# Kernel optimization log

Measured on AMD Instinct MI355X. Metric: run time of the kernel, lower is better.

## Reference

```python
import jax, jax.numpy as jnp
import numpy as np
from jax import lax

C_IN = 256
C_OUT = 256
KS = 3


def _conv(x, w, b):
    # x: [B,C,H,W], w: [O,I,kh,kw] -> NCHW 'SAME' conv, stride 1
    y = lax.conv_general_dilated(x, w, window_strides=(1, 1), padding='SAME',
                                 dimension_numbers=('NCHW', 'OIHW', 'NCHW'))
    return y + b[None, :, None, None]


def setup_inputs() -> dict:
    key = jax.random.key(0)
    ks = jax.random.split(key, 7)
    B, H, W = 2, 64, 64
    fan = C_IN * KS * KS
    lim = float(np.sqrt(6.0 / (fan + C_OUT * KS * KS)))  # xavier uniform
    return {
        'x': jax.random.normal(ks[0], (B, C_IN, H, W), jnp.float32),
        'ref_x': jax.random.normal(ks[1], (B, C_IN, H, W), jnp.float32),
        'conv1_w': jax.random.uniform(ks[2], (C_OUT, C_IN, KS, KS), jnp.float32, -lim, lim),
        'conv1_b': jnp.zeros((C_OUT,), jnp.float32),
        'conv2_w': jax.random.uniform(ks[3], (C_OUT, C_IN, KS, KS), jnp.float32, -lim, lim),
        'conv2_b': jnp.zeros((C_OUT,), jnp.float32),
        'gamma': jnp.array([0.5], jnp.float32),
    }


def reference(x, ref_x, conv1_w, conv1_b, conv2_w, conv2_b, gamma):
    B, Cin, H, W = x.shape
    HW = H * W
    x_f = jax.nn.relu(_conv(x, conv1_w, conv1_b)).reshape(B, C_OUT, HW)        # [B,C,HW]
    r_f = jax.nn.relu(_conv(ref_x, conv1_w, conv1_b))                          # [B,C,H,W]
    r_f = r_f.transpose(0, 2, 3, 1).reshape(B, HW, C_OUT)                      # [B,HW,C]
    corr = jnp.einsum('bnc,bcm->bnm', r_f, x_f)                                # [B,HW,HW]
    corr = jax.nn.softmax(corr, axis=1)                                        # softmax over ref positions
    ref_c2 = jax.nn.relu(_conv(x, conv2_w, conv2_b)).reshape(B, C_OUT, HW)     # [B,C,HW]
    A = jnp.einsum('bcn,bnm->bcm', ref_c2, corr).reshape(x.shape)              # [B,C,H,W]
    return A * gamma[0] + x
```

## Files before the change

### kernel.cpp

```cpp
#include <hip/hip_runtime.h>
#include <hip/hip_bf16.h>

#define B_ 2
#define C_ 256
#define H_ 64
#define W_ 64
#define N_ 4096

typedef short bf16x8 __attribute__((ext_vector_type(8)));
typedef _Float16 f16x8 __attribute__((ext_vector_type(8)));
typedef float f32x4 __attribute__((ext_vector_type(4)));

static __device__ __forceinline__ unsigned short f2bf(float f) {
    union { float f; unsigned u; } uf; uf.f = f;
    unsigned r = uf.u + 0x7fffu + ((uf.u >> 16) & 1u);
    return (unsigned short)(r >> 16);
}
static __device__ __forceinline__ unsigned short f2h_u(float f) {
    union { _Float16 h; unsigned short u; } c; c.h = (_Float16)f; return c.u;
}

static __device__ __forceinline__ void gload16(const void* g, void* l) {
    __builtin_amdgcn_global_load_lds(
        (const __attribute__((address_space(1))) unsigned int*)g,
        (__attribute__((address_space(3))) unsigned int*)l, 16, 0, 0);
}

__global__ __launch_bounds__(256) void cvt_x_k(const float* __restrict__ x,
                                               const float* __restrict__ ref_x,
                                               unsigned short* __restrict__ xtx,
                                               unsigned short* __restrict__ xtr)
{
    __shared__ unsigned short t[64][72];
    const int pt = blockIdx.x, ct = blockIdx.y;
    const int which = blockIdx.z >> 1, b = blockIdx.z & 1;
    const float* in = which ? ref_x : x;
    unsigned short* out = which ? xtr : xtx;
    const int a = threadIdx.x & 63, r = threadIdx.x >> 6;
    #pragma unroll
    for (int i = 0; i < 16; ++i) {
        int c = i * 4 + r;
        t[c][a] = f2h_u(in[((size_t)(b * C_ + ct * 64 + c) << 12) + pt * 64 + a]);
    }
    __syncthreads();
    #pragma unroll
    for (int i = 0; i < 16; ++i) {
        int p = i * 4 + r;
        out[((size_t)(b * N_ + pt * 64 + p) << 8) + ct * 64 + a] = t[a][p];
    }
}

__global__ __launch_bounds__(256) void cvt_w_k(const float* __restrict__ w1,
                                               const float* __restrict__ w2,
                                               unsigned short* __restrict__ wh1,
                                               unsigned short* __restrict__ wh2)
{
    int g = blockIdx.x;
    const float* w = (g < 2304) ? w1 : w2;
    unsigned short* wh = (g < 2304) ? wh1 : wh2;
    int i = (g % 2304) * 256 + threadIdx.x;
    int ci = i & 255, co = (i >> 8) & 255, tap = i >> 16;
    wh[i] = f2h_u(w[((size_t)(co * 256 + ci)) * 9 + tap]);
}

__global__ __launch_bounds__(256) void conv_mfma_k(
    const unsigned short* __restrict__ xtx, const unsigned short* __restrict__ xtr,
    const unsigned short* __restrict__ w1h, const unsigned short* __restrict__ w2h,
    const float* __restrict__ b1, const float* __restrict__ b2,
    unsigned short* __restrict__ f1x, unsigned short* __restrict__ f1r,
    unsigned short* __restrict__ f2)
{
    __shared__ unsigned short As[4 * 576 * 8];
    __shared__ unsigned short Bs[4 * 66 * 32];
    const int tid = threadIdx.x;
    const int pt  = blockIdx.x;
    const int cot = blockIdx.y;
    const int cid = blockIdx.z >> 1;
    const int b   = blockIdx.z & 1;

    const unsigned short* xt = (cid == 1) ? xtr : xtx;
    const unsigned short* wt = (cid == 2) ? w2h : w1h;
    const float* bias = (cid == 2) ? b2 : b1;
    unsigned short* out = (cid == 0) ? f1x : (cid == 1) ? f1r : f2;
    const int trans = (cid != 2);

    const int lane = tid & 63, wid = tid >> 6;
    const int wco = wid >> 1, wpos = wid & 1;
    const int rl = lane & 15, q = lane >> 4;
    const int r0 = pt * 2;

    f32x4 acc[2][4];
    #pragma unroll
    for (int mi = 0; mi < 2; ++mi)
        #pragma unroll
        for (int ni = 0; ni < 4; ++ni)
            #pragma unroll
            for (int e = 0; e < 4; ++e) acc[mi][ni][e] = 0.f;

    for (int k0 = 0; k0 < C_; k0 += 32) {
        #pragma unroll
        for (int tap = 0; tap < 9; ++tap) {
            gload16(wt + ((size_t)(tap * C_ + cot * 64 + lane) << 8) + k0 + wid * 8,
                    &As[(wid * 576 + tap * 64 + lane) * 8]);
        }
        #pragma unroll
        for (int j = 0; j < 5; ++j) {
            int it = tid + j * 256;
            if (it < 1056) {
                int col = it >> 4, sub = it & 15;
                int row = sub >> 2, qb = sub & 3;
                int h = r0 + row - 1, c = col - 1;
                float4 v; v.x = 0.f; v.y = 0.f; v.z = 0.f; v.w = 0.f;
                if (h >= 0 && h < 64 && c >= 0 && c < 64)
                    v = *(const float4*)(xt + ((size_t)(b * N_ + h * 64 + c) << 8) + k0 + qb * 8);
                int chunk = qb ^ ((col >> 1) & 3);
                *(float4*)&Bs[(row * 66 + col) * 32 + chunk * 8] = v;
            }
        }
        __syncthreads();

        #pragma unroll
        for (int tap = 0; tap < 9; ++tap) {
            const int kh = tap / 3, kw = tap % 3;
            f16x8 a0 = *(const f16x8*)&As[(q * 576 + tap * 64 + wco * 32 + rl) * 8];
            f16x8 a1 = *(const f16x8*)&As[(q * 576 + tap * 64 + wco * 32 + 16 + rl) * 8];
            const int chunkB = q ^ (((rl + kw) >> 1) & 3);
            const int rowB = (wpos + kh) * 66;
            #pragma unroll
            for (int ni = 0; ni < 4; ++ni) {
                int colB = ni * 16 + rl + kw;
                f16x8 bf = *(const f16x8*)&Bs[(rowB + colB) * 32 + chunkB * 8];
                acc[0][ni] = __builtin_amdgcn_mfma_f32_16x16x32_f16(a0, bf, acc[0][ni], 0, 0, 0);
                acc[1][ni] = __builtin_amdgcn_mfma_f32_16x16x32_f16(a1, bf, acc[1][ni], 0, 0, 0);
            }
        }
        __syncthreads();
    }

    #pragma unroll
    for (int mi = 0; mi < 2; ++mi) {
        const int co = cot * 64 + wco * 32 + mi * 16 + q * 4;
        float bs[4];
        #pragma unroll
        for (int rr = 0; rr < 4; ++rr) bs[rr] = bias[co + rr];
        #pragma unroll
        for (int ni = 0; ni < 4; ++ni) {
            const int pos = pt * 128 + wpos * 64 + ni * 16 + rl;
            if (trans) {
                unsigned short pk[4];
                #pragma unroll
                for (int rr = 0; rr < 4; ++rr)
                    pk[rr] = f2bf(fmaxf(acc[mi][ni][rr] + bs[rr], 0.f));
                uint2 u;
                u.x = (unsigned)pk[0] | ((unsigned)pk[1] << 16);
                u.y = (unsigned)pk[2] | ((unsigned)pk[3] << 16);
                *(uint2*)&out[((size_t)(b * N_ + pos) << 8) + co] = u;
            } else {
                #pragma unroll
                for (int rr = 0; rr < 4; ++rr)
                    out[((size_t)(b * C_ + co + rr) << 12) + pos] =
                        f2bf(fmaxf(acc[mi][ni][rr] + bs[rr], 0.f));
            }
        }
    }
}

__global__ __launch_bounds__(256) void gemm_corr_k(
    const unsigned short* __restrict__ f1x, const unsigned short* __restrict__ f1r,
    float* __restrict__ corr)
{
    __shared__ alignas(16) unsigned short As[128 * 32];
    __shared__ alignas(16) unsigned short Bs[128 * 32];
    const int tid = threadIdx.x;
    const int tn = blockIdx.x, tm = blockIdx.y, b = blockIdx.z;

    const unsigned short* Ab = f1x + ((size_t)b * N_ + (size_t)tm * 128) * C_;
    const unsigned short* Bb = f1r + ((size_t)b * N_ + (size_t)tn * 128) * C_;

    const int wid = tid >> 6, lane = tid & 63;
    const int wr = wid >> 1, wc = wid & 1;
    const int rl = lane & 15, q = lane >> 4;
    const int srow = wid * 32 + (lane >> 2), sq = lane & 3;

    f32x4 acc[4][4];
    #pragma unroll
    for (int mi = 0; mi < 4; ++mi)
        #pragma unroll
        for (int ni = 0; ni < 4; ++ni)
            #pragma unroll
            for (int e = 0; e < 4; ++e) acc[mi][ni][e] = 0.f;

    for (int k0 = 0; k0 < C_; k0 += 32) {
        gload16(&Ab[(size_t)srow * C_ + k0 + sq * 8],        &As[srow * 32 + sq * 8]);
        gload16(&Ab[(size_t)(srow + 16) * C_ + k0 + sq * 8], &As[(srow + 16) * 32 + sq * 8]);
        gload16(&Bb[(size_t)srow * C_ + k0 + sq * 8],        &Bs[srow * 32 + sq * 8]);
        gload16(&Bb[(size_t)(srow + 16) * C_ + k0 + sq * 8], &Bs[(srow + 16) * 32 + sq * 8]);
        __syncthreads();
        bf16x8 a[4], bb[4];
        #pragma unroll
        for (int mi = 0; mi < 4; ++mi)
            a[mi] = *(const bf16x8*)&As[(wr * 64 + mi * 16 + rl) * 32 + q * 8];
        #pragma unroll
        for (int ni = 0; ni < 4; ++ni)
            bb[ni] = *(const bf16x8*)&Bs[(wc * 64 + ni * 16 + rl) * 32 + q * 8];
        #pragma unroll
        for (int mi = 0; mi < 4; ++mi)
            #pragma unroll
            for (int ni = 0; ni < 4; ++ni)
                acc[mi][ni] = __builtin_amdgcn_mfma_f32_16x16x32_bf16(a[mi], bb[ni], acc[mi][ni], 0, 0, 0);
        __syncthreads();
    }

    #pragma unroll
    for (int mi = 0; mi < 4; ++mi)
        #pragma unroll
        for (int ni = 0; ni < 4; ++ni)
            #pragma unroll
            for (int rr = 0; rr < 4; ++rr) {
                int m = tm * 128 + wr * 64 + mi * 16 + q * 4 + rr;
                int n = tn * 128 + wc * 64 + ni * 16 + rl;
                corr[((size_t)b * N_ + m) * N_ + n] = acc[mi][ni][rr];
            }
}

__global__ __launch_bounds__(256) void softmax_rows_k(float* __restrict__ corr)
{
    __shared__ float red[4];
    const int m = blockIdx.x, b = blockIdx.y;
    float* row = corr + ((size_t)b * N_ + m) * N_;
    float4* row4 = (float4*)row;
    const int tid = threadIdx.x;
    const int wid = tid >> 6, lane = tid & 63;

    float4 v[4];
    float mx = -3.0e38f;
    #pragma unroll
    for (int j = 0; j < 4; ++j) {
        v[j] = row4[tid + j * 256];
        mx = fmaxf(mx, fmaxf(fmaxf(v[j].x, v[j].y), fmaxf(v[j].z, v[j].w)));
    }
    #pragma unroll
    for (int off = 32; off; off >>= 1) mx = fmaxf(mx, __shfl_xor(mx, off));
    if (lane == 0) red[wid] = mx;
    __syncthreads();
    mx = fmaxf(fmaxf(red[0], red[1]), fmaxf(red[2], red[3]));
    __syncthreads();

    float s = 0.f;
    #pragma unroll
    for (int j = 0; j < 4; ++j) {
        v[j].x = __expf(v[j].x - mx);
        v[j].y = __expf(v[j].y - mx);
        v[j].z = __expf(v[j].z - mx);
        v[j].w = __expf(v[j].w - mx);
        s += v[j].x + v[j].y + v[j].z + v[j].w;
    }
    #pragma unroll
    for (int off = 32; off; off >>= 1) s += __shfl_xor(s, off);
    if (lane == 0) red[wid] = s;
    __syncthreads();
    s = red[0] + red[1] + red[2] + red[3];
    const float inv = 1.f / s;

    unsigned short* rb = (unsigned short*)row;
    #pragma unroll
    for (int j = 0; j < 4; ++j) {
        uint2 u;
        u.x = (unsigned)f2bf(v[j].x * inv) | ((unsigned)f2bf(v[j].y * inv) << 16);
        u.y = (unsigned)f2bf(v[j].z * inv) | ((unsigned)f2bf(v[j].w * inv) << 16);
        *(uint2*)&rb[4 * (tid + j * 256)] = u;
    }
}

__global__ __launch_bounds__(512) void gemm_out_k(
    const unsigned short* __restrict__ f2, float* __restrict__ corr)
{
    __shared__ alignas(16) unsigned short As[128 * 32];
    __shared__ alignas(16) unsigned short Bs[128 * 32];
    const int tid = threadIdx.x;
    const int tm = blockIdx.x;
    const int tc = blockIdx.y >> 2;
    const int s  = blockIdx.y & 3;
    const int b  = blockIdx.z;

    const unsigned short* Ab = f2 + ((size_t)b * C_ + (size_t)tc * 128) * N_;
    const unsigned short* Bb = (const unsigned short*)corr
                             + ((size_t)b * N_ + (size_t)tm * 128) * 8192;

    const int wid = tid >> 6, lane = tid & 63;
    const int wc = wid >> 2, wm = wid & 3;
    const int rl = lane & 15, q = lane >> 4;
    const int srow = wid * 16 + (lane >> 2), sq = lane & 3;
    const int nbase = s * 1024;

    f32x4 acc[4][2];
    #pragma unroll
    for (int mi = 0; mi < 4; ++mi)
        #pragma unroll
        for (int ni = 0; ni < 2; ++ni)
            #pragma unroll
            for (int e = 0; e < 4; ++e) acc[mi][ni][e] = 0.f;

    for (int kk = 0; kk < 32; ++kk) {
        const int k0 = nbase + kk * 32;
        gload16(&Ab[(size_t)srow * N_ + k0 + sq * 8],   &As[srow * 32 + sq * 8]);
        gload16(&Bb[(size_t)srow * 8192 + k0 + sq * 8], &Bs[srow * 32 + sq * 8]);
        __syncthreads();
        bf16x8 a[4], bb[2];
        #pragma unroll
        for (int mi = 0; mi < 4; ++mi)
            a[mi] = *(const bf16x8*)&As[(wc * 64 + mi * 16 + rl) * 32 + q * 8];
        #pragma unroll
        for (int ni = 0; ni < 2; ++ni)
            bb[ni] = *(const bf16x8*)&Bs[(wm * 32 + ni * 16 + rl) * 32 + q * 8];
        #pragma unroll
        for (int mi = 0; mi < 4; ++mi)
            #pragma unroll
            for (int ni = 0; ni < 2; ++ni)
                acc[mi][ni] = __builtin_amdgcn_mfma_f32_16x16x32_bf16(a[mi], bb[ni], acc[mi][ni], 0, 0, 0);
        __syncthreads();
    }

    #pragma unroll
    for (int mi = 0; mi < 4; ++mi)
        #pragma unroll
        for (int ni = 0; ni < 2; ++ni)
            #pragma unroll
            for (int rr = 0; rr < 4; ++rr) {
                int c = tc * 128 + wc * 64 + mi * 16 + q * 4 + rr;
                int m = tm * 128 + wm * 32 + ni * 16 + rl;
                size_t e = (((size_t)(s * 2 + b) * C_ + c) << 12) + m;
                corr[(e >> 11) * 4096 + 2048 + (e & 2047)] = acc[mi][ni][rr];
            }
}

__global__ __launch_bounds__(256) void reduce_k(
    const float* __restrict__ corr, const float* __restrict__ x,
    const float* __restrict__ gamma, float* __restrict__ out)
{
    const float g = gamma[0];
    size_t i = (size_t)blockIdx.x * 256 + threadIdx.x;
    size_t idx = i << 2;
    float4 sum; sum.x = 0.f; sum.y = 0.f; sum.z = 0.f; sum.w = 0.f;
    #pragma unroll
    for (int sp = 0; sp < 4; ++sp) {
        size_t e = (size_t)sp * 2097152 + idx;
        float4 v = *(const float4*)&corr[(e >> 11) * 4096 + 2048 + (e & 2047)];
        sum.x += v.x; sum.y += v.y; sum.z += v.z; sum.w += v.w;
    }
    float4 xv = ((const float4*)x)[i];
    float4 o;
    o.x = sum.x * g + xv.x;
    o.y = sum.y * g + xv.y;
    o.z = sum.z * g + xv.z;
    o.w = sum.w * g + xv.w;
    ((float4*)out)[i] = o;
}

extern "C" void kernel_launch(void* const* d_in, const int* in_sizes, int n_in,
                              void* d_out, int out_size, void* d_ws, size_t ws_size,
                              hipStream_t stream) {
    const float* x     = (const float*)d_in[0];
    const float* ref_x = (const float*)d_in[1];
    const float* w1    = (const float*)d_in[2];
    const float* b1    = (const float*)d_in[3];
    const float* w2    = (const float*)d_in[4];
    const float* b2    = (const float*)d_in[5];
    const float* gamma = (const float*)d_in[6];
    float* out = (float*)d_out;

    char* ws = (char*)d_ws;
    size_t off = 0;
    auto nxt = [&](size_t bytes) {
        char* p = ws + off;
        off += (bytes + 255) & ~(size_t)255;
        return p;
    };
    unsigned short* f1x = (unsigned short*)nxt((size_t)B_ * N_ * C_ * 2);
    unsigned short* f1r = (unsigned short*)nxt((size_t)B_ * N_ * C_ * 2);
    unsigned short* f2  = (unsigned short*)nxt((size_t)B_ * N_ * C_ * 2);
    unsigned short* xtx = (unsigned short*)nxt((size_t)B_ * N_ * C_ * 2);
    unsigned short* xtr = (unsigned short*)nxt((size_t)B_ * N_ * C_ * 2);
    unsigned short* w1h = (unsigned short*)nxt((size_t)9 * C_ * C_ * 2);
    unsigned short* w2h = (unsigned short*)nxt((size_t)9 * C_ * C_ * 2);
    float* corr = (float*)nxt((size_t)B_ * N_ * N_ * 4);

    cvt_x_k<<<dim3(64, 4, 4), 256, 0, stream>>>(x, ref_x, xtx, xtr);
    cvt_w_k<<<4608, 256, 0, stream>>>(w1, w2, w1h, w2h);

    conv_mfma_k<<<dim3(32, 4, 6), 256, 0, stream>>>(xtx, xtr, w1h, w2h, b1, b2,
                                                    f1x, f1r, f2);

    gemm_corr_k<<<dim3(32, 32, B_), 256, 0, stream>>>(f1x, f1r, corr);
    softmax_rows_k<<<dim3(N_, B_), 256, 0, stream>>>(corr);
    gemm_out_k<<<dim3(32, 8, B_), 512, 0, stream>>>(f2, corr);
    reduce_k<<<2048, 256, 0, stream>>>(corr, x, gamma, out);
}
```

Baseline: 162.3 us.

## Fuse correlation, softmax and output GEMM into flash-attention kernel with split-K combine

Replaces the separate correlation GEMM, row softmax and output GEMM, which go through a large materialized correlation matrix, with one flash-style kernel. It computes S=K·Q tiles, keeps an online max and sum, and accumulates P·V in registers over split ranges of reference positions. A combine kernel merges the partial outputs using their max and sum statistics and applies gamma and the residual. This removes the B·N·N fp32 round trips through HBM. In exchange it adds per-tile exp work and partial buffers, and has only 512 blocks with non-async LDS staging.

New measurement: 150.5 us. 1.08x faster.

```diff
diff --git a/kernel.cpp b/kernel.cpp
--- a/kernel.cpp
+++ b/kernel.cpp
@@ -10,6 +10,7 @@
 typedef short bf16x8 __attribute__((ext_vector_type(8)));
 typedef _Float16 f16x8 __attribute__((ext_vector_type(8)));
 typedef float f32x4 __attribute__((ext_vector_type(4)));
+typedef float f32x16 __attribute__((ext_vector_type(16)));
 
 static __device__ __forceinline__ unsigned short f2bf(float f) {
     union { float f; unsigned u; } uf; uf.f = f;
@@ -165,195 +166,165 @@
     }
 }
 
-__global__ __launch_bounds__(256) void gemm_corr_k(
-    const unsigned short* __restrict__ f1x, const unsigned short* __restrict__ f1r,
-    float* __restrict__ corr)
-{
-    __shared__ alignas(16) unsigned short As[128 * 32];
-    __shared__ alignas(16) unsigned short Bs[128 * 32];
+__global__ __launch_bounds__(256, 2) void flash_k(
+    const unsigned short* __restrict__ f1x,
+    const unsigned short* __restrict__ f1r,
+    const unsigned short* __restrict__ f2,
+    float* __restrict__ part,
+    float* __restrict__ stats)
+{
+    __shared__ unsigned short Ks[64 * 264];
+    __shared__ unsigned short Vs[256 * 72];
     const int tid = threadIdx.x;
-    const int tn = blockIdx.x, tm = blockIdx.y, b = blockIdx.z;
-
-    const unsigned short* Ab = f1x + ((size_t)b * N_ + (size_t)tm * 128) * C_;
-    const unsigned short* Bb = f1r + ((size_t)b * N_ + (size_t)tn * 128) * C_;
-
-    const int wid = tid >> 6, lane = tid & 63;
-    const int wr = wid >> 1, wc = wid & 1;
-    const int rl = lane & 15, q = lane >> 4;
-    const int srow = wid * 32 + (lane >> 2), sq = lane & 3;
-
-    f32x4 acc[4][4];
-    #pragma unroll
-    for (int mi = 0; mi < 4; ++mi)
-        #pragma unroll
-        for (int ni = 0; ni < 4; ++ni)
+    const int mt = blockIdx.x, s = blockIdx.y, b = blockIdx.z;
+    const int m0 = mt * 32;
+    const int lane = tid & 63, wid = tid >> 6;
+    const int wn = wid & 1, wc2 = wid >> 1;
+    const int rl = lane & 31, l5 = lane >> 5;
+    const int c0w = wc2 * 128;
+    const int nw = wn * 32;
+
+    bf16x8 Qf[16];
+    #pragma unroll
+    for (int st = 0; st < 16; ++st)
+        Qf[st] = *(const bf16x8*)&f1x[(((size_t)b * N_ + m0 + rl) << 8) + st * 16 + l5 * 8];
+
+    f32x16 O[4];
+    #pragma unroll
+    for (int cf = 0; cf < 4; ++cf)
+        #pragma unroll
+        for (int e = 0; e < 16; ++e) O[cf][e] = 0.f;
+    float m_run = -1e30f, l_run = 0.f;
+
+    const int nbase = s * 2048;
+    for (int r = 0; r < 32; ++r) {
+        const int n0 = nbase + r * 64;
+        #pragma unroll
+        for (int j = 0; j < 8; ++j) {
+            int it = tid + j * 256;
+            int n = it >> 5, cq = it & 31;
+            *(float4*)&Ks[n * 264 + cq * 8] =
+                *(const float4*)&f1r[(((size_t)b * N_ + n0 + n) << 8) + cq * 8];
+        }
+        #pragma unroll
+        for (int j = 0; j < 8; ++j) {
+            int it = tid + j * 256;
+            int c = it >> 3, nq = it & 7;
+            *(float4*)&Vs[c * 72 + nq * 8] =
+                *(const float4*)&f2[(((size_t)b * C_ + c) << 12) + n0 + nq * 8];
+        }
+        __syncthreads();
+
+        f32x16 S;
+        #pragma unroll
+        for (int e = 0; e < 16; ++e) S[e] = 0.f;
+        #pragma unroll
+        for (int st = 0; st < 16; ++st) {
+            bf16x8 Kf = *(const bf16x8*)&Ks[(nw + rl) * 264 + st * 16 + l5 * 8];
+            S = __builtin_amdgcn_mfma_f32_32x32x16_bf16(Kf, Qf[st], S, 0, 0, 0);
+        }
+
+        float mx = S[0];
+        #pragma unroll
+        for (int e = 1; e < 16; ++e) mx = fmaxf(mx, S[e]);
+        mx = fmaxf(mx, __shfl_xor(mx, 32));
+        float m_new = fmaxf(m_run, mx);
+        float sc = __expf(m_run - m_new);
+        float p[16]; float lsum = 0.f;
+        #pragma unroll
+        for (int e = 0; e < 16; ++e) { p[e] = __expf(S[e] - m_new); lsum += p[e]; }
+        l_run = l_run * sc + lsum;
+        m_run = m_new;
+        #pragma unroll
+        for (int cf = 0; cf < 4; ++cf)
             #pragma unroll
-            for (int e = 0; e < 4; ++e) acc[mi][ni][e] = 0.f;
-
-    for (int k0 = 0; k0 < C_; k0 += 32) {
-        gload16(&Ab[(size_t)srow * C_ + k0 + sq * 8],        &As[srow * 32 + sq * 8]);
-        gload16(&Ab[(size_t)(srow + 16) * C_ + k0 + sq * 8], &As[(srow + 16) * 32 + sq * 8]);
-        gload16(&Bb[(size_t)srow * C_ + k0 + sq * 8],        &Bs[srow * 32 + sq * 8]);
-        gload16(&Bb[(size_t)(srow + 16) * C_ + k0 + sq * 8], &Bs[(srow + 16) * 32 + sq * 8]);
+            for (int e = 0; e < 16; ++e) O[cf][e] *= sc;
+
+        unsigned pk_[8], xk[8];
+        #pragma unroll
+        for (int g = 0; g < 8; ++g)
+            pk_[g] = (unsigned)f2bf(p[2 * g]) | ((unsigned)f2bf(p[2 * g + 1]) << 16);
+        #pragma unroll
+        for (int g = 0; g < 8; ++g) xk[g] = (unsigned)__shfl_xor((int)pk_[g], 32);
+        union { unsigned d[4]; bf16x8 v; } P0, P1;
+        P0.d[0] = l5 ? xk[2] : pk_[0];
+        P0.d[1] = l5 ? xk[3] : pk_[1];
+        P0.d[2] = l5 ? pk_[2] : xk[0];
+        P0.d[3] = l5 ? pk_[3] : xk[1];
+        P1.d[0] = l5 ? xk[6] : pk_[4];
+        P1.d[1] = l5 ? xk[7] : pk_[5];
+        P1.d[2] = l5 ? pk_[6] : xk[4];
+        P1.d[3] = l5 ? pk_[7] : xk[5];
+
+        #pragma unroll
+        for (int cf = 0; cf < 4; ++cf) {
+            const int vrow = (c0w + cf * 32 + rl) * 72;
+            bf16x8 Vf0 = *(const bf16x8*)&Vs[vrow + nw + l5 * 8];
+            O[cf] = __builtin_amdgcn_mfma_f32_32x32x16_bf16(Vf0, P0.v, O[cf], 0, 0, 0);
+            bf16x8 Vf1 = *(const bf16x8*)&Vs[vrow + nw + 16 + l5 * 8];
+            O[cf] = __builtin_amdgcn_mfma_f32_32x32x16_bf16(Vf1, P1.v, O[cf], 0, 0, 0);
+        }
         __syncthreads();
-        bf16x8 a[4], bb[4];
-        #pragma unroll
-        for (int mi = 0; mi < 4; ++mi)
-            a[mi] = *(const bf16x8*)&As[(wr * 64 + mi * 16 + rl) * 32 + q * 8];
-        #pragma unroll
-        for (int ni = 0; ni < 4; ++ni)
-            bb[ni] = *(const bf16x8*)&Bs[(wc * 64 + ni * 16 + rl) * 32 + q * 8];
-        #pragma unroll
-        for (int mi = 0; mi < 4; ++mi)
-            #pragma unroll
-            for (int ni = 0; ni < 4; ++ni)
-                acc[mi][ni] = __builtin_amdgcn_mfma_f32_16x16x32_bf16(a[mi], bb[ni], acc[mi][ni], 0, 0, 0);
-        __syncthreads();
-    }
-
-    #pragma unroll
-    for (int mi = 0; mi < 4; ++mi)
-        #pragma unroll
-        for (int ni = 0; ni < 4; ++ni)
-            #pragma unroll
-            for (int rr = 0; rr < 4; ++rr) {
-                int m = tm * 128 + wr * 64 + mi * 16 + q * 4 + rr;
-                int n = tn * 128 + wc * 64 + ni * 16 + rl;
-                corr[((size_t)b * N_ + m) * N_ + n] = acc[mi][ni][rr];
-            }
-}
-
-__global__ __launch_bounds__(256) void softmax_rows_k(float* __restrict__ corr)
-{
-    __shared__ float red[4];
-    const int m = blockIdx.x, b = blockIdx.y;
-    float* row = corr + ((size_t)b * N_ + m) * N_;
-    float4* row4 = (float4*)row;
-    const int tid = threadIdx.x;
-    const int wid = tid >> 6, lane = tid & 63;
-
-    float4 v[4];
-    float mx = -3.0e38f;
-    #pragma unroll
-    for (int j = 0; j < 4; ++j) {
-        v[j] = row4[tid + j * 256];
-        mx = fmaxf(mx, fmaxf(fmaxf(v[j].x, v[j].y), fmaxf(v[j].z, v[j].w)));
-    }
-    #pragma unroll
-    for (int off = 32; off; off >>= 1) mx = fmaxf(mx, __shfl_xor(mx, off));
-    if (lane == 0) red[wid] = mx;
-    __syncthreads();
-    mx = fmaxf(fmaxf(red[0], red[1]), fmaxf(red[2], red[3]));
-    __syncthreads();
-
-    float s = 0.f;
-    #pragma unroll
-    for (int j = 0; j < 4; ++j) {
-        v[j].x = __expf(v[j].x - mx);
-        v[j].y = __expf(v[j].y - mx);
-        v[j].z = __expf(v[j].z - mx);
-        v[j].w = __expf(v[j].w - mx);
-        s += v[j].x + v[j].y + v[j].z + v[j].w;
-    }
-    #pragma unroll
-    for (int off = 32; off; off >>= 1) s += __shfl_xor(s, off);
-    if (lane == 0) red[wid] = s;
-    __syncthreads();
-    s = red[0] + red[1] + red[2] + red[3];
-    const float inv = 1.f / s;
-
-    unsigned short* rb = (unsigned short*)row;
-    #pragma unroll
-    for (int j = 0; j < 4; ++j) {
-        uint2 u;
-        u.x = (unsigned)f2bf(v[j].x * inv) | ((unsigned)f2bf(v[j].y * inv) << 16);
-        u.y = (unsigned)f2bf(v[j].z * inv) | ((unsigned)f2bf(v[j].w * inv) << 16);
-        *(uint2*)&rb[4 * (tid + j * 256)] = u;
-    }
-}
-
-__global__ __launch_bounds__(512) void gemm_out_k(
-    const unsigned short* __restrict__ f2, float* __restrict__ corr)
-{
-    __shared__ alignas(16) unsigned short As[128 * 32];
-    __shared__ alignas(16) unsigned short Bs[128 * 32];
-    const int tid = threadIdx.x;
-    const int tm = blockIdx.x;
-    const int tc = blockIdx.y >> 2;
-    const int s  = blockIdx.y & 3;
-    const int b  = blockIdx.z;
-
-    const unsigned short* Ab = f2 + ((size_t)b * C_ + (size_t)tc * 128) * N_;
-    const unsigned short* Bb = (const unsigned short*)corr
-                             + ((size_t)b * N_ + (size_t)tm * 128) * 8192;
-
-    const int wid = tid >> 6, lane = tid & 63;
-    const int wc = wid >> 2, wm = wid & 3;
-    const int rl = lane & 15, q = lane >> 4;
-    const int srow = wid * 16 + (lane >> 2), sq = lane & 3;
-    const int nbase = s * 1024;
-
-    f32x4 acc[4][2];
-    #pragma unroll
-    for (int mi = 0; mi < 4; ++mi)
-        #pragma unroll
-        for (int ni = 0; ni < 2; ++ni)
-            #pragma unroll
-            for (int e = 0; e < 4; ++e) acc[mi][ni][e] = 0.f;
-
-    for (int kk = 0; kk < 32; ++kk) {
-        const int k0 = nbase + kk * 32;
-        gload16(&Ab[(size_t)srow * N_ + k0 + sq * 8],   &As[srow * 32 + sq * 8]);
-        gload16(&Bb[(size_t)srow * 8192 + k0 + sq * 8], &Bs[srow * 32 + sq * 8]);
-        __syncthreads();
-        bf16x8 a[4], bb[2];
-        #pragma unroll
-        for (int mi = 0; mi < 4; ++mi)
-            a[mi] = *(const bf16x8*)&As[(wc * 64 + mi * 16 + rl) * 32 + q * 8];
-        #pragma unroll
-        for (int ni = 0; ni < 2; ++ni)
-            bb[ni] = *(const bf16x8*)&Bs[(wm * 32 + ni * 16 + rl) * 32 + q * 8];
-        #pragma unroll
-        for (int mi = 0; mi < 4; ++mi)
-            #pragma unroll
-            for (int ni = 0; ni < 2; ++ni)
-                acc[mi][ni] = __builtin_amdgcn_mfma_f32_16x16x32_bf16(a[mi], bb[ni], acc[mi][ni], 0, 0, 0);
-        __syncthreads();
-    }
-
-    #pragma unroll
-    for (int mi = 0; mi < 4; ++mi)
-        #pragma unroll
-        for (int ni = 0; ni < 2; ++ni)
-            #pragma unroll
-            for (int rr = 0; rr < 4; ++rr) {
-                int c = tc * 128 + wc * 64 + mi * 16 + q * 4 + rr;
-                int m = tm * 128 + wm * 32 + ni * 16 + rl;
-                size_t e = (((size_t)(s * 2 + b) * C_ + c) << 12) + m;
-                corr[(e >> 11) * 4096 + 2048 + (e & 2047)] = acc[mi][ni][rr];
-            }
-}
-
-__global__ __launch_bounds__(256) void reduce_k(
-    const float* __restrict__ corr, const float* __restrict__ x,
-    const float* __restrict__ gamma, float* __restrict__ out)
+    }
+
+    float l_tot = l_run + __shfl_xor(l_run, 32);
+    const int se = s * 2 + wn;
+    float* pb = part + (size_t)se * ((size_t)B_ * C_ * N_);
+    #pragma unroll
+    for (int cf = 0; cf < 4; ++cf)
+        #pragma unroll
+        for (int e = 0; e < 16; ++e) {
+            int c = c0w + cf * 32 + (e & 3) + 8 * (e >> 2) + 4 * l5;
+            pb[(((size_t)b * C_ + c) << 12) + m0 + rl] = O[cf][e];
+        }
+    if (wc2 == 0 && l5 == 0) {
+        float2 st; st.x = m_run; st.y = l_tot;
+        ((float2*)stats)[(((size_t)(se * 2 + b)) << 12) + m0 + rl] = st;
+    }
+}
+
+__global__ __launch_bounds__(256) void combine_k(
+    const float* __restrict__ part, const float* __restrict__ stats,
+    const float* __restrict__ x, const float* __restrict__ gamma,
+    float* __restrict__ out)
 {
     const float g = gamma[0];
     size_t i = (size_t)blockIdx.x * 256 + threadIdx.x;
     size_t idx = i << 2;
-    float4 sum; sum.x = 0.f; sum.y = 0.f; sum.z = 0.f; sum.w = 0.f;
-    #pragma unroll
-    for (int sp = 0; sp < 4; ++sp) {
-        size_t e = (size_t)sp * 2097152 + idx;
-        float4 v = *(const float4*)&corr[(e >> 11) * 4096 + 2048 + (e & 2047)];
-        sum.x += v.x; sum.y += v.y; sum.z += v.z; sum.w += v.w;
+    const int m = (int)(idx & 4095);
+    const int b = (int)(idx >> 20);
+    const size_t PS = (size_t)B_ * C_ * N_;
+
+    float ms[4][4], ls[4][4];
+    #pragma unroll
+    for (int se = 0; se < 4; ++se) {
+        const float2* sp = (const float2*)stats + (((size_t)(se * 2 + b)) << 12) + m;
+        #pragma unroll
+        for (int j = 0; j < 4; ++j) { float2 v = sp[j]; ms[se][j] = v.x; ls[se][j] = v.y; }
+    }
+    float w[4][4], den[4] = {0.f, 0.f, 0.f, 0.f};
+    #pragma unroll
+    for (int j = 0; j < 4; ++j) {
+        float M = fmaxf(fmaxf(ms[0][j], ms[1][j]), fmaxf(ms[2][j], ms[3][j]));
+        #pragma unroll
+        for (int se = 0; se < 4; ++se) {
+            w[se][j] = __expf(ms[se][j] - M);
+            den[j] += w[se][j] * ls[se][j];
+        }
+    }
+    float num[4] = {0.f, 0.f, 0.f, 0.f};
+    #pragma unroll
+    for (int se = 0; se < 4; ++se) {
+        float4 p = *(const float4*)&part[se * PS + idx];
+        num[0] += w[se][0] * p.x; num[1] += w[se][1] * p.y;
+        num[2] += w[se][2] * p.z; num[3] += w[se][3] * p.w;
     }
     float4 xv = ((const float4*)x)[i];
     float4 o;
-    o.x = sum.x * g + xv.x;
-    o.y = sum.y * g + xv.y;
-    o.z = sum.z * g + xv.z;
-    o.w = sum.w * g + xv.w;
+    o.x = g * num[0] / den[0] + xv.x;
+    o.y = g * num[1] / den[1] + xv.y;
+    o.z = g * num[2] / den[2] + xv.z;
+    o.w = g * num[3] / den[3] + xv.w;
     ((float4*)out)[i] = o;
 }
 
@@ -383,7 +354,8 @@
     unsigned short* xtr = (unsigned short*)nxt((size_t)B_ * N_ * C_ * 2);
     unsigned short* w1h = (unsigned short*)nxt((size_t)9 * C_ * C_ * 2);
     unsigned short* w2h = (unsigned short*)nxt((size_t)9 * C_ * C_ * 2);
-    float* corr = (float*)nxt((size_t)B_ * N_ * N_ * 4);
+    float* part  = (float*)nxt((size_t)4 * B_ * C_ * N_ * 4);
+    float* stats = (float*)nxt((size_t)4 * B_ * N_ * 8);
 
     cvt_x_k<<<dim3(64, 4, 4), 256, 0, stream>>>(x, ref_x, xtx, xtr);
     cvt_w_k<<<4608, 256, 0, stream>>>(w1, w2, w1h, w2h);
@@ -391,8 +363,6 @@
     conv_mfma_k<<<dim3(32, 4, 6), 256, 0, stream>>>(xtx, xtr, w1h, w2h, b1, b2,
                                                     f1x, f1r, f2);
 
-    gemm_corr_k<<<dim3(32, 32, B_), 256, 0, stream>>>(f1x, f1r, corr);
-    softmax_rows_k<<<dim3(N_, B_), 256, 0, stream>>>(corr);
-    gemm_out_k<<<dim3(32, 8, B_), 512, 0, stream>>>(f2, corr);
-    reduce_k<<<2048, 256, 0, stream>>>(corr, x, gamma, out);
-}
+    flash_k<<<dim3(128, 2, 2), 256, 0, stream>>>(f1x, f1r, f2, part, stats);
+    combine_k<<<2048, 256, 0, stream>>>(part, stats, x, gamma, out);
+}
```
